# Performance work log

Hardware: AMD Instinct MI355X
Metric: run time of the kernel (lower is better)

## Reference

```python
import jax, jax.numpy as jnp
import numpy as np

EPS = 1e-12


def t5_layer_norm(x, w):
    # RMS norm without mean subtraction (T5 style)
    var = jnp.mean(x * x, axis=-1, keepdims=True)
    return w * (x * jax.lax.rsqrt(var + EPS))


def gether(h, a_simi, t_simi, adj):
    # h: [B,S,S,D]; a_simi/t_simi: [B,S]; adj: [B,S,S]
    diag = jnp.einsum('bssd->bsd', h)                 # h[b,l,l,:]
    h_adj = jnp.einsum('bld,blk->blkd', diag, adj)    # diag broadcast by adjacency
    h_y = h * t_simi[:, None, :, None]                # t_simi varies along axis 2
    h_x = h * a_simi[:, :, None, None]                # a_simi varies along axis 1
    h_left = jnp.pad(h_y, ((0, 0), (0, 0), (1, 0), (0, 0)))[:, :, :-1, :]
    h_right = jnp.pad(h_y, ((0, 0), (0, 0), (0, 1), (0, 0)))[:, :, 1:, :]
    h_up = jnp.pad(h_x, ((0, 0), (1, 0), (0, 0), (0, 0)))[:, :-1, :, :]
    h_down = jnp.pad(h_x, ((0, 0), (0, 1), (0, 0), (0, 0)))[:, 1:, :, :]
    return h + h_adj + h_left + h_right + h_up + h_down


def setup_inputs() -> dict:
    key = jax.random.key(0)
    ks = jax.random.split(key, 10)
    B, S, D_in, D_out = 8, 96, 768, 256
    table = jax.random.normal(ks[0], (B, S, S, D_in), dtype=jnp.float32)
    a_simi = jax.random.uniform(ks[1], (B, S), dtype=jnp.float32)
    t_simi = jax.random.uniform(ks[2], (B, S), dtype=jnp.float32)
    adj_matrix = jax.random.uniform(ks[3], (B, S, S), dtype=jnp.float32)
    s1 = 1.0 / np.sqrt(D_in)
    W1 = jax.random.uniform(ks[4], (D_in, D_in), jnp.float32, -s1, s1)
    b1 = jax.random.uniform(ks[5], (D_in,), jnp.float32, -s1, s1)
    g1 = jnp.ones((D_in,), jnp.float32)
    W2 = jax.random.uniform(ks[6], (D_in, D_out), jnp.float32, -s1, s1)
    b2 = jax.random.uniform(ks[7], (D_out,), jnp.float32, -s1, s1)
    g2 = jnp.ones((D_out,), jnp.float32)
    return {"table": table, "a_simi": a_simi, "t_simi": t_simi,
            "adj_matrix": adj_matrix, "W1": W1, "b1": b1, "g1": g1,
            "W2": W2, "b2": b2, "g2": g2}


def reference(table, a_simi, t_simi, adj_matrix, W1, b1, g1, W2, b2, g2):
    h0 = table
    h1 = gether(h0, a_simi, t_simi, adj_matrix)
    h1 = jax.nn.relu(t5_layer_norm((h1 + h0) @ W1 + b1, g1))
    h2 = gether(h1, a_simi, t_simi, adj_matrix)
    h2 = jax.nn.relu(t5_layer_norm((h2 + h1) @ W2 + b2, g2))
    return h2
```

## Files before the change

kernel.cpp:

```cpp
#include <hip/hip_runtime.h>

typedef __bf16 bf16;
typedef __bf16 bf16x4 __attribute__((ext_vector_type(4)));
typedef __bf16 bf16x8 __attribute__((ext_vector_type(8)));
typedef float f32x4 __attribute__((ext_vector_type(4)));
typedef float floatx4 __attribute__((ext_vector_type(4)));

#define S 96
#define DIN 768
#define DOUT 256
#define MROWS 73728

__device__ static inline void async16(const bf16* g, bf16* l) {
    __builtin_amdgcn_global_load_lds(
        (const __attribute__((address_space(1))) void*)g,
        (__attribute__((address_space(3))) void*)l,
        16, 0, 0);
}

__global__ __launch_bounds__(256) void k_gether1(
    const float* __restrict__ H, const float* __restrict__ Asim,
    const float* __restrict__ Tsim, const float* __restrict__ Adj,
    bf16* __restrict__ X)
{
    __shared__ float adjs[S];
    __shared__ float ts[S];
    __shared__ float diagf[DIN];
    int bx = blockIdx.x;
    bx = (bx & 7) * (gridDim.x >> 3) + (bx >> 3);
    int b = bx / S, l = bx % S;
    int tid = threadIdx.x;
    long row0 = (long)(b * S + l) * S;
    if (tid < S) {
        adjs[tid] = Adj[(b * S + l) * S + tid];
        ts[tid]   = Tsim[b * S + tid];
    }
    for (int i = tid; i < DIN / 4; i += 256)
        *(f32x4*)&diagf[i * 4] = *(const f32x4*)&H[(row0 + l) * DIN + i * 4];
    float a_up = (l > 0)     ? Asim[b * S + l - 1] : 0.f;
    float a_dn = (l < S - 1) ? Asim[b * S + l + 1] : 0.f;
    long du = (l > 0)     ? -(long)S * DIN : 0;
    long dd = (l < S - 1) ?  (long)S * DIN : 0;
    __syncthreads();

    int lane = tid & 63, wv = tid >> 6;
    int k0 = blockIdx.y * (S / 2);
    for (int k = k0 + wv; k < k0 + S / 2; k += 4) {
        float tl = (k > 0)     ? ts[k - 1] : 0.f;
        float tr = (k < S - 1) ? ts[k + 1] : 0.f;
        long  dl = (k > 0)     ? -(long)DIN : 0;
        long  dr = (k < S - 1) ?  (long)DIN : 0;
        float aj = adjs[k];
        const float* hrow = H + (row0 + k) * DIN;
        bf16* xrow = X + (row0 + k) * DIN;
#pragma unroll
        for (int c = 0; c < 3; ++c) {
            int col = (lane + c * 64) * 4;
            const float* hc = hrow + col;
            f32x4 vc = *(const f32x4*)hc;
            f32x4 vl = *(const f32x4*)(hc + dl);
            f32x4 vr = *(const f32x4*)(hc + dr);
            f32x4 vu = *(const f32x4*)(hc + du);
            f32x4 vd = *(const f32x4*)(hc + dd);
            bf16x4 o;
#pragma unroll
            for (int j = 0; j < 4; ++j) {
                float v = 2.f * vc[j] + aj * diagf[col + j]
                        + tl * vl[j] + tr * vr[j]
                        + a_up * vu[j] + a_dn * vd[j];
                o[j] = (bf16)v;
            }
            *(bf16x4*)&xrow[col] = o;
        }
    }
}

__global__ __launch_bounds__(256) void k_gether2(
    const bf16* __restrict__ Y, const float* __restrict__ INV,
    const float* __restrict__ G1, const float* __restrict__ Asim,
    const float* __restrict__ Tsim, const float* __restrict__ Adj,
    bf16* __restrict__ X)
{
    __shared__ float adjs[S];
    __shared__ float ts[S];
    __shared__ float diagf[DIN];
    __shared__ float g1s[DIN];
    int bx = blockIdx.x;
    bx = (bx & 7) * (gridDim.x >> 3) + (bx >> 3);
    int b = bx / S, l = bx % S;
    int tid = threadIdx.x;
    long row0 = (long)(b * S + l) * S;
    for (int i = tid; i < DIN; i += 256) g1s[i] = G1[i];
    __syncthreads();
    if (tid < S) {
        adjs[tid] = Adj[(b * S + l) * S + tid];
        ts[tid]   = Tsim[b * S + tid];
        float iv = INV[row0 + l];
        bf16x8 yv = *(const bf16x8*)&Y[(row0 + l) * DIN + tid * 8];
#pragma unroll
        for (int j = 0; j < 8; ++j) {
            float v = g1s[tid * 8 + j] * (float)yv[j] * iv;
            diagf[tid * 8 + j] = v > 0.f ? v : 0.f;
        }
    }
    float a_up = (l > 0)     ? Asim[b * S + l - 1] : 0.f;
    float a_dn = (l < S - 1) ? Asim[b * S + l + 1] : 0.f;
    long du = (l > 0)     ? -(long)S * DIN : 0;
    long dd = (l < S - 1) ?  (long)S * DIN : 0;
    int ou = (l > 0) ? -S : 0;
    int od = (l < S - 1) ? S : 0;
    __syncthreads();

    int lane = tid & 63, wv = tid >> 6;
    int k0 = blockIdx.y * (S / 2);
    for (int k = k0 + wv; k < k0 + S / 2; k += 4) {
        float tl = (k > 0)     ? ts[k - 1] : 0.f;
        float tr = (k < S - 1) ? ts[k + 1] : 0.f;
        int   ol = (k > 0)     ? -1 : 0;
        int   orr = (k < S - 1) ? 1 : 0;
        float aj = adjs[k];
        float ivc = INV[row0 + k];
        float ivl = INV[row0 + k + ol];
        float ivr = INV[row0 + k + orr];
        float ivu = INV[row0 + k + ou];
        float ivd = INV[row0 + k + od];
        const bf16* yrow = Y + (row0 + k) * DIN;
        bf16* xrow = X + (row0 + k) * DIN;
#pragma unroll
        for (int c = 0; c < 3; ++c) {
            int col = (lane + c * 64) * 4;
            const bf16* yc = yrow + col;
            bf16x4 vc = *(const bf16x4*)yc;
            bf16x4 vl = *(const bf16x4*)(yc + (long)ol * DIN);
            bf16x4 vr = *(const bf16x4*)(yc + (long)orr * DIN);
            bf16x4 vu = *(const bf16x4*)(yc + du);
            bf16x4 vd = *(const bf16x4*)(yc + dd);
            bf16x4 o;
#pragma unroll
            for (int j = 0; j < 4; ++j) {
                float g = g1s[col + j];
                float hc_ = g * (float)vc[j] * ivc; hc_ = hc_ > 0.f ? hc_ : 0.f;
                float hl_ = g * (float)vl[j] * ivl; hl_ = hl_ > 0.f ? hl_ : 0.f;
                float hr_ = g * (float)vr[j] * ivr; hr_ = hr_ > 0.f ? hr_ : 0.f;
                float hu_ = g * (float)vu[j] * ivu; hu_ = hu_ > 0.f ? hu_ : 0.f;
                float hd_ = g * (float)vd[j] * ivd; hd_ = hd_ > 0.f ? hd_ : 0.f;
                float v = 2.f * hc_ + aj * diagf[col + j]
                        + tl * hl_ + tr * hr_ + a_up * hu_ + a_dn * hd_;
                o[j] = (bf16)v;
            }
            *(bf16x4*)&xrow[col] = o;
        }
    }
}

__global__ __launch_bounds__(256) void k_gemm1(
    const bf16* __restrict__ Xm, const bf16* __restrict__ WT,
    const float* __restrict__ bias, bf16* __restrict__ Y,
    float* __restrict__ ssq)
{
    constexpr int K = 768, N = 768;
    constexpr int NT = K / 32;
    __shared__ __align__(16) bf16 As[3][128 * 32];
    __shared__ __align__(16) bf16 Bs[3][128 * 32];
    int t = threadIdx.x;
    int wg = blockIdx.x;
    wg = (wg & 7) * (gridDim.x >> 3) + (wg >> 3);
    int colBase = (wg % 6) * 128;
    int rowBase = (wg / 6) * 128;
    int lane = t & 63, w = t >> 6;
    int quad = lane >> 4, l16 = lane & 15;
    int wr = w >> 1, wc = w & 1;

    floatx4 acc[4][4];
#pragma unroll
    for (int i = 0; i < 4; ++i)
#pragma unroll
        for (int j = 0; j < 4; ++j) acc[i][j] = (floatx4)0.f;

    int chunk = (t & 3) ^ ((t >> 3) & 3);
    const bf16* gA = Xm + (size_t)(rowBase + (t >> 2)) * K + chunk * 8;
    const bf16* gB = WT + (size_t)(colBase + (t >> 2)) * K + chunk * 8;
    int l8 = t * 8;

    auto stage = [&](int buf, int kk) {
        async16(gA + kk, &As[buf][l8]);
        async16(gA + kk + 64 * K, &As[buf][l8 + 2048]);
        async16(gB + kk, &Bs[buf][l8]);
        async16(gB + kk + 64 * K, &Bs[buf][l8 + 2048]);
    };

    stage(0, 0);
    stage(1, 32);
    for (int tt = 0; tt < NT; ++tt) {
        if (tt + 1 < NT) asm volatile("s_waitcnt vmcnt(4)" ::: "memory");
        else             asm volatile("s_waitcnt vmcnt(0)" ::: "memory");
        __builtin_amdgcn_s_barrier();
        int cur = tt % 3;
        bf16x8 af[4], bfr[4];
#pragma unroll
        for (int i = 0; i < 4; ++i) {
            int ra = wr * 64 + i * 16 + l16;
            af[i] = *(const bf16x8*)&As[cur][ra * 32 + (quad ^ ((ra >> 1) & 3)) * 8];
        }
#pragma unroll
        for (int j = 0; j < 4; ++j) {
            int rb = wc * 64 + j * 16 + l16;
            bfr[j] = *(const bf16x8*)&Bs[cur][rb * 32 + (quad ^ ((rb >> 1) & 3)) * 8];
        }
        if (tt + 2 < NT) stage((tt + 2) % 3, (tt + 2) * 32);
#pragma unroll
        for (int i = 0; i < 4; ++i)
#pragma unroll
            for (int j = 0; j < 4; ++j)
                acc[i][j] = __builtin_amdgcn_mfma_f32_16x16x32_bf16(
                    af[i], bfr[j], acc[i][j], 0, 0, 0);
    }

    float bv[4];
#pragma unroll
    for (int j = 0; j < 4; ++j)
        bv[j] = bias[colBase + wc * 64 + j * 16 + l16];
#pragma unroll
    for (int i = 0; i < 4; ++i) {
#pragma unroll
        for (int r = 0; r < 4; ++r) {
            int row = rowBase + wr * 64 + i * 16 + quad * 4 + r;
            bf16* yp = Y + (size_t)row * N + colBase + wc * 64 + l16;
            float s = 0.f;
#pragma unroll
            for (int j = 0; j < 4; ++j) {
                float v = acc[i][j][r] + bv[j];
                s += v * v;
                yp[j * 16] = (bf16)v;
            }
            s += __shfl_xor(s, 1);
            s += __shfl_xor(s, 2);
            s += __shfl_xor(s, 4);
            s += __shfl_xor(s, 8);
            if (l16 == 0) atomicAdd(&ssq[row], s);
        }
    }
}

__global__ __launch_bounds__(256, 2) void k_gemm2f(
    const bf16* __restrict__ Xm, const bf16* __restrict__ WT,
    const float* __restrict__ bias, const float* __restrict__ G2,
    float* __restrict__ out)
{
    constexpr int K = 768, N = 256;
    constexpr int NT = K / 32;
    __shared__ __align__(16) bf16 As[3][128 * 32];
    __shared__ __align__(16) bf16 Bs[3][256 * 32];
    __shared__ float ssqs[2][128];
    int t = threadIdx.x;
    int rowBase = blockIdx.x * 128;
    int lane = t & 63, w = t >> 6;
    int quad = lane >> 4, l16 = lane & 15;
    int wr = w >> 1, wc = w & 1;

    floatx4 acc[4][8];
#pragma unroll
    for (int i = 0; i < 4; ++i)
#pragma unroll
        for (int j = 0; j < 8; ++j) acc[i][j] = (floatx4)0.f;

    int chunk = (t & 3) ^ ((t >> 3) & 3);
    const bf16* gA = Xm + (size_t)(rowBase + (t >> 2)) * K + chunk * 8;
    const bf16* gB = WT + (size_t)(t >> 2) * K + chunk * 8;
    int l8 = t * 8;

    auto stage = [&](int buf, int kk) {
        async16(gA + kk, &As[buf][l8]);
        async16(gA + kk + 64 * K, &As[buf][l8 + 2048]);
        async16(gB + kk, &Bs[buf][l8]);
        async16(gB + kk + 64 * K, &Bs[buf][l8 + 2048]);
        async16(gB + kk + 128 * K, &Bs[buf][l8 + 4096]);
        async16(gB + kk + 192 * K, &Bs[buf][l8 + 6144]);
    };

    stage(0, 0);
    stage(1, 32);
    for (int tt = 0; tt < NT; ++tt) {
        if (tt + 1 < NT) asm volatile("s_waitcnt vmcnt(6)" ::: "memory");
        else             asm volatile("s_waitcnt vmcnt(0)" ::: "memory");
        __builtin_amdgcn_s_barrier();
        int cur = tt % 3;
        bf16x8 af[4], bfr[8];
#pragma unroll
        for (int i = 0; i < 4; ++i) {
            int ra = wr * 64 + i * 16 + l16;
            af[i] = *(const bf16x8*)&As[cur][ra * 32 + (quad ^ ((ra >> 1) & 3)) * 8];
        }
#pragma unroll
        for (int j = 0; j < 8; ++j) {
            int rb = wc * 128 + j * 16 + l16;
            bfr[j] = *(const bf16x8*)&Bs[cur][rb * 32 + (quad ^ ((rb >> 1) & 3)) * 8];
        }
        if (tt + 2 < NT) stage((tt + 2) % 3, (tt + 2) * 32);
#pragma unroll
        for (int i = 0; i < 4; ++i)
#pragma unroll
            for (int j = 0; j < 8; ++j)
                acc[i][j] = __builtin_amdgcn_mfma_f32_16x16x32_bf16(
                    af[i], bfr[j], acc[i][j], 0, 0, 0);
    }

    float bv[8], gv[8];
#pragma unroll
    for (int j = 0; j < 8; ++j) {
        int col = wc * 128 + j * 16 + l16;
        bv[j] = bias[col];
        gv[j] = G2[col];
    }
#pragma unroll
    for (int i = 0; i < 4; ++i) {
#pragma unroll
        for (int r = 0; r < 4; ++r) {
            float s = 0.f;
#pragma unroll
            for (int j = 0; j < 8; ++j) {
                float v = acc[i][j][r] + bv[j];
                s += v * v;
            }
            s += __shfl_xor(s, 1);
            s += __shfl_xor(s, 2);
            s += __shfl_xor(s, 4);
            s += __shfl_xor(s, 8);
            if (l16 == 0)
                ssqs[wc][wr * 64 + i * 16 + quad * 4 + r] = s;
        }
    }
    __syncthreads();
#pragma unroll
    for (int i = 0; i < 4; ++i) {
#pragma unroll
        for (int r = 0; r < 4; ++r) {
            int lr = wr * 64 + i * 16 + quad * 4 + r;
            float inv = rsqrtf((ssqs[0][lr] + ssqs[1][lr]) * (1.f / N) + 1e-12f);
            float* op = out + (size_t)(rowBase + lr) * N + wc * 128 + l16;
#pragma unroll
            for (int j = 0; j < 8; ++j) {
                float v = (acc[i][j][r] + bv[j]) * gv[j] * inv;
                op[j * 16] = v > 0.f ? v : 0.f;
            }
        }
    }
}

__global__ __launch_bounds__(256) void k_invr(float* ssq, int n, float invD)
{
    int i = blockIdx.x * 256 + threadIdx.x;
    if (i < n) ssq[i] = rsqrtf(ssq[i] * invD + 1e-12f);
}

__global__ __launch_bounds__(256) void k_castT(
    const float* __restrict__ in, bf16* __restrict__ out, int R, int C)
{
    __shared__ float tile[32][33];
    int lx = threadIdx.x & 31, ly = threadIdx.x >> 5;
    int c0 = blockIdx.x * 32, r0 = blockIdx.y * 32;
#pragma unroll
    for (int k = 0; k < 4; ++k)
        tile[ly + 8 * k][lx] = in[(size_t)(r0 + ly + 8 * k) * C + c0 + lx];
    __syncthreads();
#pragma unroll
    for (int k = 0; k < 4; ++k)
        out[(size_t)(c0 + ly + 8 * k) * R + r0 + lx] = (bf16)tile[lx][ly + 8 * k];
}

extern "C" void kernel_launch(void* const* d_in, const int* in_sizes, int n_in,
                              void* d_out, int out_size, void* d_ws, size_t ws_size,
                              hipStream_t stream)
{
    const float* table = (const float*)d_in[0];
    const float* asim  = (const float*)d_in[1];
    const float* tsim  = (const float*)d_in[2];
    const float* adj   = (const float*)d_in[3];
    const float* W1    = (const float*)d_in[4];
    const float* b1    = (const float*)d_in[5];
    const float* g1    = (const float*)d_in[6];
    const float* W2    = (const float*)d_in[7];
    const float* b2    = (const float*)d_in[8];
    const float* g2    = (const float*)d_in[9];
    float* out = (float*)d_out;

    char* ws = (char*)d_ws;
    const size_t SZ_X = (size_t)MROWS * DIN * 2;
    bf16*  X    = (bf16*)ws;
    bf16*  Y1   = (bf16*)(ws + SZ_X);
    bf16*  W1T  = (bf16*)(ws + 2 * SZ_X);
    bf16*  W2T  = (bf16*)(ws + 2 * SZ_X + 1179648);
    float* ssq1 = (float*)(ws + 2 * SZ_X + 1179648 + 393216);

    hipMemsetAsync(ssq1, 0, (size_t)MROWS * 4, stream);
    k_castT<<<dim3(DIN / 32, DIN / 32), 256, 0, stream>>>(W1, W1T, DIN, DIN);
    k_castT<<<dim3(DOUT / 32, DIN / 32), 256, 0, stream>>>(W2, W2T, DIN, DOUT);

    k_gether1<<<dim3(8 * S, 2), 256, 0, stream>>>(table, asim, tsim, adj, X);
    k_gemm1<<<dim3((DIN / 128) * (MROWS / 128)), 256, 0, stream>>>(X, W1T, b1, Y1, ssq1);
    k_invr<<<MROWS / 256, 256, 0, stream>>>(ssq1, MROWS, 1.f / DIN);
    k_gether2<<<dim3(8 * S, 2), 256, 0, stream>>>(Y1, ssq1, g1, asim, tsim, adj, X);
    k_gemm2f<<<MROWS / 128, 256, 0, stream>>>(X, W2T, b2, g2, out);
}
```

Baseline: 636.0 us.

## Enlarge gemm1 to 256x256 tiles with 8 waves and interleaved prefetch

Rewrites the first GEMM to use 256x256 output tiles, 512 threads (8 waves, each computing 128x64), and BK=64 with double-buffered LDS. Global-to-LDS loads for the next k-tile are spread across four sub-phases and interleaved with MFMA blocks, using barriers, setprio and a new XOR swizzle. The aim is to raise arithmetic intensity and cut redundant global loads of X and W, and to overlap loads with compute. In exchange it uses 128KB of LDS per block and many more accumulator registers, which limits occupancy. It also adds extra barriers per k-step.

```diff
diff --git a/kernel.cpp b/kernel.cpp
--- a/kernel.cpp
+++ b/kernel.cpp
@@ -153,67 +153,93 @@
     }
 }
 
-__global__ __launch_bounds__(256) void k_gemm1(
+__global__ __launch_bounds__(512, 2) void k_gemm1(
     const bf16* __restrict__ Xm, const bf16* __restrict__ WT,
     const float* __restrict__ bias, bf16* __restrict__ Y,
     float* __restrict__ ssq)
 {
     constexpr int K = 768, N = 768;
-    constexpr int NT = K / 32;
-    __shared__ __align__(16) bf16 As[3][128 * 32];
-    __shared__ __align__(16) bf16 Bs[3][128 * 32];
+    constexpr int NTILE = K / 64;
+    __shared__ __align__(16) bf16 As[2][256 * 64];
+    __shared__ __align__(16) bf16 Bs[2][256 * 64];
     int t = threadIdx.x;
     int wg = blockIdx.x;
     wg = (wg & 7) * (gridDim.x >> 3) + (wg >> 3);
-    int colBase = (wg % 6) * 128;
-    int rowBase = (wg / 6) * 128;
+    int colBase = (wg % 3) * 256;
+    int rowBase = (wg / 3) * 256;
     int lane = t & 63, w = t >> 6;
     int quad = lane >> 4, l16 = lane & 15;
-    int wr = w >> 1, wc = w & 1;
-
-    floatx4 acc[4][4];
-#pragma unroll
-    for (int i = 0; i < 4; ++i)
+    int wr = w >> 2, wc = w & 3;
+
+    floatx4 acc[8][4];
+#pragma unroll
+    for (int i = 0; i < 8; ++i)
 #pragma unroll
         for (int j = 0; j < 4; ++j) acc[i][j] = (floatx4)0.f;
 
-    int chunk = (t & 3) ^ ((t >> 3) & 3);
-    const bf16* gA = Xm + (size_t)(rowBase + (t >> 2)) * K + chunk * 8;
-    const bf16* gB = WT + (size_t)(colBase + (t >> 2)) * K + chunk * 8;
-    int l8 = t * 8;
-
-    auto stage = [&](int buf, int kk) {
-        async16(gA + kk, &As[buf][l8]);
-        async16(gA + kk + 64 * K, &As[buf][l8 + 2048]);
-        async16(gB + kk, &Bs[buf][l8]);
-        async16(gB + kk + 64 * K, &Bs[buf][l8 + 2048]);
+    int tr = t >> 3;
+    int gc = (t & 7) ^ (tr & 7);
+    const bf16* gA = Xm + (size_t)(rowBase + tr) * K + gc * 8;
+    const bf16* gB = WT + (size_t)(colBase + tr) * K + gc * 8;
+    int ldst = t * 8;
+
+    auto stageA = [&](int b, int s, int kt) {
+        async16(gA + (size_t)s * 64 * K + kt * 64, &As[b][s * 4096 + ldst]);
     };
-
-    stage(0, 0);
-    stage(1, 32);
-    for (int tt = 0; tt < NT; ++tt) {
-        if (tt + 1 < NT) asm volatile("s_waitcnt vmcnt(4)" ::: "memory");
-        else             asm volatile("s_waitcnt vmcnt(0)" ::: "memory");
-        __builtin_amdgcn_s_barrier();
-        int cur = tt % 3;
-        bf16x8 af[4], bfr[4];
-#pragma unroll
-        for (int i = 0; i < 4; ++i) {
-            int ra = wr * 64 + i * 16 + l16;
-            af[i] = *(const bf16x8*)&As[cur][ra * 32 + (quad ^ ((ra >> 1) & 3)) * 8];
-        }
-#pragma unroll
-        for (int j = 0; j < 4; ++j) {
-            int rb = wc * 64 + j * 16 + l16;
-            bfr[j] = *(const bf16x8*)&Bs[cur][rb * 32 + (quad ^ ((rb >> 1) & 3)) * 8];
-        }
-        if (tt + 2 < NT) stage((tt + 2) % 3, (tt + 2) * 32);
-#pragma unroll
-        for (int i = 0; i < 4; ++i)
+    auto stageB = [&](int b, int s, int kt) {
+        async16(gB + (size_t)s * 64 * K + kt * 64, &Bs[b][s * 4096 + ldst]);
+    };
+
+    stageB(0, 0, 0); stageB(0, 1, 0); stageB(0, 2, 0); stageB(0, 3, 0);
+    stageA(0, 0, 0); stageA(0, 2, 0); stageA(0, 1, 0); stageA(0, 3, 0);
+    asm volatile("s_waitcnt vmcnt(2)" ::: "memory");
+    __builtin_amdgcn_s_barrier();
+
+    int swz = l16 & 7;
+    int cK0 = (quad ^ swz) * 8;
+    int cK1 = ((quad + 4) ^ swz) * 8;
+
+    for (int tt = 0; tt < NTILE; ++tt) {
+        int cur = tt & 1;
+        int nb = cur ^ 1;
+        bool more = (tt + 1 < NTILE);
+        const bf16* aB = &As[cur][(wr * 128 + l16) * 64];
+        const bf16* bB = &Bs[cur][(wc * 64 + l16) * 64];
+#pragma unroll
+        for (int p = 0; p < 4; ++p) {
+            const int ihalf = p & 1;
+            const int co = (p >> 1) ? cK1 : cK0;
+            bf16x8 af[4], bfr[4];
+#pragma unroll
+            for (int ii = 0; ii < 4; ++ii)
+                af[ii] = *(const bf16x8*)(aB + (ihalf * 4 + ii) * 1024 + co);
 #pragma unroll
             for (int j = 0; j < 4; ++j)
-                acc[i][j] = __builtin_amdgcn_mfma_f32_16x16x32_bf16(
-                    af[i], bfr[j], acc[i][j], 0, 0, 0);
+                bfr[j] = *(const bf16x8*)(bB + j * 1024 + co);
+            if (more) {
+                if (p == 0) { stageB(nb, 0, tt + 1); stageB(nb, 1, tt + 1); }
+                if (p == 1) { stageB(nb, 2, tt + 1); stageB(nb, 3, tt + 1); }
+                if (p == 2) { stageA(nb, 0, tt + 1); stageA(nb, 2, tt + 1); }
+                if (p == 3) { stageA(nb, 1, tt + 1); stageA(nb, 3, tt + 1); }
+            }
+            __builtin_amdgcn_s_barrier();
+            asm volatile("s_waitcnt lgkmcnt(0)" ::: "memory");
+            __builtin_amdgcn_sched_barrier(0);
+            __builtin_amdgcn_s_setprio(1);
+#pragma unroll
+            for (int ii = 0; ii < 4; ++ii)
+#pragma unroll
+                for (int j = 0; j < 4; ++j)
+                    acc[ihalf * 4 + ii][j] = __builtin_amdgcn_mfma_f32_16x16x32_bf16(
+                        af[ii], bfr[j], acc[ihalf * 4 + ii][j], 0, 0, 0);
+            __builtin_amdgcn_s_setprio(0);
+            if (p == 0) {
+                if (more) asm volatile("s_waitcnt vmcnt(2)" ::: "memory");
+                else      asm volatile("s_waitcnt vmcnt(0)" ::: "memory");
+            }
+            if (p == 3 && more) asm volatile("s_waitcnt vmcnt(2)" ::: "memory");
+            __builtin_amdgcn_s_barrier();
+        }
     }
 
     float bv[4];
@@ -221,10 +247,10 @@
     for (int j = 0; j < 4; ++j)
         bv[j] = bias[colBase + wc * 64 + j * 16 + l16];
 #pragma unroll
-    for (int i = 0; i < 4; ++i) {
+    for (int i = 0; i < 8; ++i) {
 #pragma unroll
         for (int r = 0; r < 4; ++r) {
-            int row = rowBase + wr * 64 + i * 16 + quad * 4 + r;
+            int row = rowBase + wr * 128 + i * 16 + quad * 4 + r;
             bf16* yp = Y + (size_t)row * N + colBase + wc * 64 + l16;
             float s = 0.f;
 #pragma unroll
@@ -397,7 +423,7 @@
     k_castT<<<dim3(DOUT / 32, DIN / 32), 256, 0, stream>>>(W2, W2T, DIN, DOUT);
 
     k_gether1<<<dim3(8 * S, 2), 256, 0, stream>>>(table, asim, tsim, adj, X);
-    k_gemm1<<<dim3((DIN / 128) * (MROWS / 128)), 256, 0, stream>>>(X, W1T, b1, Y1, ssq1);
+    k_gemm1<<<dim3((DIN / 256) * (MROWS / 256)), 512, 0, stream>>>(X, W1T, b1, Y1, ssq1);
     k_invr<<<MROWS / 256, 256, 0, stream>>>(ssq1, MROWS, 1.f / DIN);
     k_gether2<<<dim3(8 * S, 2), 256, 0, stream>>>(Y1, ssq1, g1, asim, tsim, adj, X);
     k_gemm2f<<<MROWS / 128, 256, 0, stream>>>(X, W2T, b2, g2, out);
```

Result: no change. 637.6 us (+0.3%).
